# Kernel tuning notes

Hardware: AMD Instinct MI355X
Metric: run time of the kernel (lower is better)

## Reference

```python
import jax, jax.numpy as jnp
import numpy as np

B, S, H, NH = 1, 4096, 1024, 16
HD = H // NH  # 64


def _rope_tables(seq_len, dim):
    inv_freq = 1.0 / (10000.0 ** (np.arange(0, dim, 2, dtype=np.float32) / dim))
    t = np.arange(seq_len, dtype=np.float32)
    freqs = np.outer(t, inv_freq)                 # [S, dim/2]
    emb = np.concatenate([freqs, freqs], axis=-1)  # [S, dim]
    return jnp.asarray(np.cos(emb)), jnp.asarray(np.sin(emb))


def setup_inputs() -> dict:
    key = jax.random.key(0)
    ks = jax.random.split(key, 5)
    hidden_states = jax.random.normal(ks[0], (B, S, H), dtype=jnp.float32)
    scale = 1.0 / np.sqrt(H)
    Wq = jax.random.normal(ks[1], (H, H), dtype=jnp.float32) * scale
    Wk = jax.random.normal(ks[2], (H, H), dtype=jnp.float32) * scale
    Wv = jax.random.normal(ks[3], (H, H), dtype=jnp.float32) * scale
    Wo = jax.random.normal(ks[4], (H, H), dtype=jnp.float32) * scale
    cos, sin = _rope_tables(S, HD)
    # additive causal mask [1,1,S,S]
    causal = jnp.where(
        jnp.tril(jnp.ones((S, S), dtype=bool)), 0.0, jnp.float32(-1e9)
    )[None, None]
    return {
        "hidden_states": hidden_states,
        "cos": cos,
        "sin": sin,
        "attention_mask": causal,
        "Wq": Wq,
        "Wk": Wk,
        "Wv": Wv,
        "Wo": Wo,
    }


def _rotate_half(x):
    x1, x2 = jnp.split(x, 2, axis=-1)
    return jnp.concatenate([-x2, x1], axis=-1)


def _apply_rope(q, k, cos, sin):
    # q,k: [B,NH,S,HD]; cos/sin: [S,HD] -> broadcast [1,1,S,HD]
    cos = cos[None, None]
    sin = sin[None, None]
    q = q * cos + _rotate_half(q) * sin
    k = k * cos + _rotate_half(k) * sin
    return q, k


def reference(hidden_states, cos, sin, attention_mask, Wq, Wk, Wv, Wo):
    bsz, q_len, _ = hidden_states.shape
    q = hidden_states @ Wq.T
    k = hidden_states @ Wk.T
    v = hidden_states @ Wv.T
    # [B,S,H] -> [B,NH,S,HD]
    def split_heads(x):
        return x.reshape(bsz, q_len, NH, HD).transpose(0, 2, 1, 3)
    q, k, v = split_heads(q), split_heads(k), split_heads(v)
    q, k = _apply_rope(q, k, cos, sin)
    scores = jnp.einsum("bhqd,bhkd->bhqk", q, k) / jnp.sqrt(jnp.float32(HD))
    scores = scores + attention_mask
    attn = jax.nn.softmax(scores, axis=-1)
    out = jnp.einsum("bhqk,bhkd->bhqd", attn, v)
    out = out.transpose(0, 2, 1, 3).reshape(bsz, q_len, H)
    return out @ Wo.T
```

## Files before the change

kernel.cpp:

```cpp
#include <hip/hip_runtime.h>

#define S_LEN 4096
#define NHEADS 16
#define HD 64
#define HDIM 1024

typedef __attribute__((ext_vector_type(8))) __bf16 bf16x8;
typedef __attribute__((ext_vector_type(4))) float f32x4;
typedef __attribute__((ext_vector_type(4))) int i32x4;
typedef unsigned short u16;

static __device__ __forceinline__ u16 f2bu(float f) {
    unsigned u = __builtin_bit_cast(unsigned, f);
    u += 0x7FFFu + ((u >> 16) & 1u);
    return (u16)(u >> 16);
}
static __device__ __forceinline__ int pack_bf16(float lo, float hi) {
    return (int)__builtin_amdgcn_perm(__builtin_bit_cast(unsigned, hi),
                                      __builtin_bit_cast(unsigned, lo), 0x07060302u);
}
static __device__ __forceinline__ float fexp2(float x) {
    return __builtin_amdgcn_exp2f(x);
}

static __device__ __forceinline__ bf16x8 read_frag(const u16* lds, int row, int kbyte) {
    int c = kbyte ^ ((row & 7) << 4);
    return *reinterpret_cast<const bf16x8*>(reinterpret_cast<const char*>(lds) + row * 128 + c);
}
static __device__ __forceinline__ bf16x8 read_off(const u16* lds, int byteoff) {
    return *reinterpret_cast<const bf16x8*>(reinterpret_cast<const char*>(lds) + byteoff);
}

static __device__ __forceinline__ void stage_gll(const u16* __restrict__ src, const u16* lds, unsigned ldsbyte) {
    __builtin_amdgcn_global_load_lds(
        (const __attribute__((address_space(1))) void*)src,
        (__attribute__((address_space(3))) void*)(reinterpret_cast<const char*>(lds) + ldsbyte),
        16, 0, 0);
}

static __device__ __forceinline__ void softmax_gather(
    const f32x4* sf, float& l_part, bf16x8* pf, int lj, int lc)
{
    int pk[4][2];
#pragma unroll
    for (int nf = 0; nf < 4; ++nf) {
        float p0 = fexp2(sf[nf][0]);
        float p1 = fexp2(sf[nf][1]);
        float p2 = fexp2(sf[nf][2]);
        float p3 = fexp2(sf[nf][3]);
        l_part += (p0 + p1) + (p2 + p3);
        pk[nf][0] = pack_bf16(p0, p1);
        pk[nf][1] = pack_bf16(p2, p3);
    }
#pragma unroll
    for (int kb = 0; kb < 2; ++kb) {
        i32x4 u;
#pragma unroll
        for (int s = 0; s < 4; ++s) {
            int srcl = lc + (((2 * lj + (s >> 1)) & 3) << 4);
            int v0 = __shfl(pk[2 * kb][s & 1], srcl);
            int v1 = __shfl(pk[2 * kb + 1][s & 1], srcl);
            u[s] = (lj & 2) ? v1 : v0;
        }
        pf[kb] = __builtin_bit_cast(bf16x8, u);
    }
}

__global__ __launch_bounds__(256) void cvt_all(
    const float* __restrict__ X, const float* __restrict__ Wq, const float* __restrict__ Wk,
    const float* __restrict__ Wv, const float* __restrict__ Wo,
    u16* __restrict__ Xb, u16* __restrict__ Wqb, u16* __restrict__ Wkb,
    u16* __restrict__ Wvb, u16* __restrict__ Wob)
{
    int i = blockIdx.x * 256 + threadIdx.x;
    const float* src; u16* dst; int off;
    if (i < (1 << 20)) { src = X; dst = Xb; off = i; }
    else {
        int j = i - (1 << 20);
        int w = j >> 18; off = j & 0x3FFFF;
        src = (w == 0) ? Wq : (w == 1) ? Wk : (w == 2) ? Wv : Wo;
        dst = (w == 0) ? Wqb : (w == 1) ? Wkb : (w == 2) ? Wvb : Wob;
    }
    float4 v = reinterpret_cast<const float4*>(src)[off];
    ushort4 o;
    o.x = f2bu(v.x); o.y = f2bu(v.y); o.z = f2bu(v.z); o.w = f2bu(v.w);
    reinterpret_cast<ushort4*>(dst)[off] = o;
}

__global__ __launch_bounds__(256) void qkv_gemm(
    const u16* __restrict__ A,
    const u16* __restrict__ Wq, const u16* __restrict__ Wk, const u16* __restrict__ Wv,
    u16* __restrict__ Qb, u16* __restrict__ Kb, u16* __restrict__ VTb,
    const float* __restrict__ cosT, const float* __restrict__ sinT)
{
    __shared__ u16 At[128 * 64];
    __shared__ u16 Bt[128 * 64];
    const int z = blockIdx.z;
    const u16* W = (z == 0) ? Wq : (z == 1) ? Wk : Wv;
    const int tid = threadIdx.x;
    const int wid = tid >> 6, lane = tid & 63;
    const int wm = wid >> 1, wn = wid & 1;
    const int lj = lane >> 4, lc = lane & 15;
    const int m0 = blockIdx.y * 128, n0 = blockIdx.x * 128;

    f32x4 acc[4][4];
#pragma unroll
    for (int i = 0; i < 4; ++i)
#pragma unroll
        for (int j = 0; j < 4; ++j) acc[i][j] = 0.0f;

    for (int k0 = 0; k0 < HDIM; k0 += 64) {
        __syncthreads();
#pragma unroll
        for (int r = 0; r < 4; ++r) {
            int idx = (r << 8) + tid;
            int row = idx >> 3;
            int c = (idx & 7) << 4;
            int csw = c ^ ((row & 7) << 4);
            unsigned lb = (unsigned)(idx & ~63) << 4;
            stage_gll(A + (size_t)(m0 + row) * HDIM + k0 + (csw >> 1), At, lb);
            stage_gll(W + (size_t)(n0 + row) * HDIM + k0 + (csw >> 1), Bt, lb);
        }
        __syncthreads();
#pragma unroll
        for (int kb = 0; kb < 2; ++kb) {
            int kbyte = (kb << 6) + (lj << 4);
            bf16x8 af[4], bfr[4];
#pragma unroll
            for (int mf = 0; mf < 4; ++mf) af[mf] = read_frag(At, (wm << 6) + (mf << 4) + lc, kbyte);
#pragma unroll
            for (int nf = 0; nf < 4; ++nf) bfr[nf] = read_frag(Bt, (wn << 6) + (nf << 4) + lc, kbyte);
#pragma unroll
            for (int mf = 0; mf < 4; ++mf)
#pragma unroll
                for (int nf = 0; nf < 4; ++nf)
                    acc[mf][nf] = __builtin_amdgcn_mfma_f32_16x16x32_bf16(af[mf], bfr[nf], acc[mf][nf], 0, 0, 0);
        }
    }

    const int mrow0 = m0 + (wm << 6);
    const int ncol0 = n0 + (wn << 6);
    if (z == 2) {
#pragma unroll
        for (int mf = 0; mf < 4; ++mf)
#pragma unroll
            for (int nf = 0; nf < 4; ++nf)
#pragma unroll
                for (int j = 0; j < 4; ++j) {
                    int s = mrow0 + (mf << 4) + (lj << 2) + j;
                    int o = ncol0 + (nf << 4) + lc;
                    VTb[((size_t)(o >> 6) * HD + (o & 63)) * S_LEN + s] = f2bu(acc[mf][nf][j]);
                }
    } else {
        u16* outB = (z == 0) ? Qb : Kb;
        const float sc = (z == 0) ? 0.18033688011112042f : 1.0f;
#pragma unroll
        for (int mf = 0; mf < 4; ++mf) {
            float nv[4][4];
#pragma unroll
            for (int nf = 0; nf < 4; ++nf)
#pragma unroll
                for (int j = 0; j < 4; ++j) {
                    int s = mrow0 + (mf << 4) + (lj << 2) + j;
                    int o = ncol0 + (nf << 4) + lc;
                    int d = o & 63;
                    float x  = acc[mf][nf][j];
                    float xp = acc[mf][nf ^ 2][j];
                    float cv = cosT[(size_t)s * HD + d];
                    float sv = sinT[(size_t)s * HD + d];
                    float rot = (d < 32) ? -xp : xp;
                    nv[nf][j] = (x * cv + rot * sv) * sc;
                }
#pragma unroll
            for (int nf = 0; nf < 4; ++nf)
#pragma unroll
                for (int j = 0; j < 4; ++j) {
                    int s = mrow0 + (mf << 4) + (lj << 2) + j;
                    int o = ncol0 + (nf << 4) + lc;
                    outB[((size_t)(o >> 6) * S_LEN + s) * HD + (o & 63)] = f2bu(nv[nf][j]);
                }
        }
    }
}

__global__ __launch_bounds__(256) void wo_gemm(
    const u16* __restrict__ A, const u16* __restrict__ W, float* __restrict__ outF)
{
    __shared__ u16 At[128 * 64];
    __shared__ u16 Bt[64 * 64];
    const int tid = threadIdx.x;
    const int wid = tid >> 6, lane = tid & 63;
    const int wm = wid >> 1, wn = wid & 1;
    const int lj = lane >> 4, lc = lane & 15;
    const int m0 = blockIdx.y * 128, n0 = blockIdx.x * 64;

    f32x4 acc[4][2];
#pragma unroll
    for (int i = 0; i < 4; ++i)
#pragma unroll
        for (int j = 0; j < 2; ++j) acc[i][j] = 0.0f;

    for (int k0 = 0; k0 < HDIM; k0 += 64) {
        __syncthreads();
#pragma unroll
        for (int r = 0; r < 4; ++r) {
            int idx = (r << 8) + tid;
            int row = idx >> 3;
            int c = (idx & 7) << 4;
            int csw = c ^ ((row & 7) << 4);
            unsigned lb = (unsigned)(idx & ~63) << 4;
            stage_gll(A + (size_t)(m0 + row) * HDIM + k0 + (csw >> 1), At, lb);
            if (r < 2)
                stage_gll(W + (size_t)(n0 + row) * HDIM + k0 + (csw >> 1), Bt, lb);
        }
        __syncthreads();
#pragma unroll
        for (int kb = 0; kb < 2; ++kb) {
            int kbyte = (kb << 6) + (lj << 4);
            bf16x8 af[4], bfr[2];
#pragma unroll
            for (int mf = 0; mf < 4; ++mf) af[mf] = read_frag(At, (wm << 6) + (mf << 4) + lc, kbyte);
#pragma unroll
            for (int nf = 0; nf < 2; ++nf) bfr[nf] = read_frag(Bt, (wn << 5) + (nf << 4) + lc, kbyte);
#pragma unroll
            for (int mf = 0; mf < 4; ++mf)
#pragma unroll
                for (int nf = 0; nf < 2; ++nf)
                    acc[mf][nf] = __builtin_amdgcn_mfma_f32_16x16x32_bf16(af[mf], bfr[nf], acc[mf][nf], 0, 0, 0);
        }
    }

    const int mrow0 = m0 + (wm << 6);
    const int ncol0 = n0 + (wn << 5);
#pragma unroll
    for (int mf = 0; mf < 4; ++mf)
#pragma unroll
        for (int nf = 0; nf < 2; ++nf)
#pragma unroll
            for (int j = 0; j < 4; ++j) {
                int s = mrow0 + (mf << 4) + (lj << 2) + j;
                int o = ncol0 + (nf << 4) + lc;
                outF[(size_t)s * HDIM + o] = acc[mf][nf][j];
            }
}

__global__ __launch_bounds__(256, 2) void attn_fwd(
    const u16* __restrict__ Q, const u16* __restrict__ K,
    const u16* __restrict__ VT, u16* __restrict__ AO)
{
    __shared__ u16 Kt[2][128 * 64];
    __shared__ u16 Vt[2][2][64 * 64];

    const int tid = threadIdx.x;
    const int wid = tid >> 6, lane = tid & 63;
    const int lj = lane >> 4, lc = lane & 15;

    const int lid = blockIdx.x;
    const int x = lid & 7, g = lid >> 3;
    const int a = g >> 5, c = g & 31;
    const int b = a ? (31 - c) : c;
    const int h = (x << 1) | a;
    const int qtA = 63 - b, qtB = b;
    const int qbaseA = qtA * 64 + wid * 16;
    const int qbaseB = qtB * 64 + wid * 16;
    const int nsteps = qtA + 1;

    const u16* Qh = Q + (size_t)h * S_LEN * HD;

    const int srow = tid >> 3;
    const int csw  = ((tid & 7) << 4) ^ ((srow & 7) << 4);
    const u16* kbase = K  + (size_t)h * S_LEN * HD + (size_t)srow * HD + (csw >> 1);
    const u16* vbase = VT + (size_t)h * HD * S_LEN + (size_t)srow * S_LEN + (csw >> 1);
    const unsigned lb = (unsigned)(tid & ~63) << 4;

#define SK(buf, hf, t) do { \
        const u16* p_ = kbase + (size_t)(t) * 64 * HD; \
        stage_gll(p_,           (const u16*)Kt[buf] + (hf) * 4096, lb); \
        stage_gll(p_ + 32 * HD, (const u16*)Kt[buf] + (hf) * 4096, lb + 4096); \
    } while (0)
#define SV(buf, hf, t) do { \
        const u16* p_ = vbase + (t) * 64; \
        stage_gll(p_,              (const u16*)Vt[buf][hf], lb); \
        stage_gll(p_ + 32 * S_LEN, (const u16*)Vt[buf][hf], lb + 4096); \
    } while (0)

    int foff[2][4];
#pragma unroll
    for (int kb = 0; kb < 2; ++kb)
#pragma unroll
        for (int nf = 0; nf < 4; ++nf) {
            int row = (nf << 4) + lc;
            foff[kb][nf] = row * 128 + (((kb << 6) + (lj << 4)) ^ ((row & 7) << 4));
        }

    bf16x8 qB0[2], qB1[2];
#pragma unroll
    for (int kb = 0; kb < 2; ++kb) {
        qB0[kb] = *reinterpret_cast<const bf16x8*>(
            Qh + (size_t)(qbaseA + lc) * HD + (kb << 5) + (lj << 3));
        qB1[kb] = *reinterpret_cast<const bf16x8*>(
            Qh + (size_t)(qbaseB + lc) * HD + (kb << 5) + (lj << 3));
    }

    f32x4 accO0[4], accO1[4];
    float l0 = 0.0f, l1 = 0.0f;
#pragma unroll
    for (int df = 0; df < 4; ++df) { accO0[df] = 0.0f; accO1[df] = 0.0f; }

    bf16x8 pf0[2], pf1[2], vf[2][4];

    auto compute = [&](int t, const u16* KtH, const u16* VtH) {
        const bool act1 = (t <= qtB);
        const bool pv1  = (t >= 1) && (t <= qtB + 1);

        bf16x8 kf[2][4];
#pragma unroll
        for (int kb = 0; kb < 2; ++kb)
#pragma unroll
            for (int nf = 0; nf < 4; ++nf)
                kf[kb][nf] = read_off(KtH, foff[kb][nf]);

        f32x4 sf0[4], sf1[4];
#pragma unroll
        for (int nf = 0; nf < 4; ++nf) { sf0[nf] = 0.0f; sf1[nf] = 0.0f; }

        __builtin_amdgcn_s_setprio(1);
#pragma unroll
        for (int kb = 0; kb < 2; ++kb)
#pragma unroll
            for (int nf = 0; nf < 4; ++nf)
                sf0[nf] = __builtin_amdgcn_mfma_f32_16x16x32_bf16(kf[kb][nf], qB0[kb], sf0[nf], 0, 0, 0);
        if (act1) {
#pragma unroll
            for (int kb = 0; kb < 2; ++kb)
#pragma unroll
                for (int nf = 0; nf < 4; ++nf)
                    sf1[nf] = __builtin_amdgcn_mfma_f32_16x16x32_bf16(kf[kb][nf], qB1[kb], sf1[nf], 0, 0, 0);
        }
        if (t >= 1) {
#pragma unroll
            for (int kb = 0; kb < 2; ++kb)
#pragma unroll
                for (int df = 0; df < 4; ++df)
                    accO0[df] = __builtin_amdgcn_mfma_f32_16x16x32_bf16(pf0[kb], vf[kb][df], accO0[df], 0, 0, 0);
        }
        if (pv1) {
#pragma unroll
            for (int kb = 0; kb < 2; ++kb)
#pragma unroll
                for (int df = 0; df < 4; ++df)
                    accO1[df] = __builtin_amdgcn_mfma_f32_16x16x32_bf16(pf1[kb], vf[kb][df], accO1[df], 0, 0, 0);
        }
        __builtin_amdgcn_s_setprio(0);

#pragma unroll
        for (int kb = 0; kb < 2; ++kb)
#pragma unroll
            for (int df = 0; df < 4; ++df)
                vf[kb][df] = read_off(VtH, foff[kb][df]);

        const int kv0 = t << 6;
        if (t == qtA) {
            int qg = qbaseA + lc;
#pragma unroll
            for (int nf = 0; nf < 4; ++nf)
#pragma unroll
                for (int j = 0; j < 4; ++j) {
                    int kvg = kv0 + (nf << 4) + (lj << 2) + j;
                    if (kvg > qg) sf0[nf][j] = -1e30f;
                }
        }
        if (act1 && t == qtB) {
            int qg = qbaseB + lc;
#pragma unroll
            for (int nf = 0; nf < 4; ++nf)
#pragma unroll
                for (int j = 0; j < 4; ++j) {
                    int kvg = kv0 + (nf << 4) + (lj << 2) + j;
                    if (kvg > qg) sf1[nf][j] = -1e30f;
                }
        }

        softmax_gather(sf0, l0, pf0, lj, lc);
        if (act1) softmax_gather(sf1, l1, pf1, lj, lc);
    };

    SK(0, 0, 0); SV(0, 0, 0);
    if (nsteps > 1) { SK(0, 1, 1); SV(0, 1, 1); }
    __syncthreads();

    const int nmac = (nsteps + 1) >> 1;
    int cur = 0;
    for (int m = 0; m < nmac; ++m) {
        const int t2 = 2 * m + 2, t3 = 2 * m + 3;
        if (t2 < nsteps) { SK(cur ^ 1, 0, t2); SV(cur ^ 1, 0, t2); }
        if (t3 < nsteps) { SK(cur ^ 1, 1, t3); SV(cur ^ 1, 1, t3); }

        compute(2 * m, (const u16*)Kt[cur], (const u16*)Vt[cur][0]);
        if (2 * m + 1 < nsteps)
            compute(2 * m + 1, (const u16*)Kt[cur] + 4096, (const u16*)Vt[cur][1]);

        __syncthreads();
        cur ^= 1;
    }

#pragma unroll
    for (int kb = 0; kb < 2; ++kb)
#pragma unroll
        for (int df = 0; df < 4; ++df)
            accO0[df] = __builtin_amdgcn_mfma_f32_16x16x32_bf16(pf0[kb], vf[kb][df], accO0[df], 0, 0, 0);

    l0 += __shfl_xor(l0, 16); l0 += __shfl_xor(l0, 32);
    l1 += __shfl_xor(l1, 16); l1 += __shfl_xor(l1, 32);
    float lr0[4], lr1[4];
#pragma unroll
    for (int j = 0; j < 4; ++j) {
        lr0[j] = __shfl(l0, (lj << 2) + j);
        lr1[j] = __shfl(l1, (lj << 2) + j);
    }
#pragma unroll
    for (int df = 0; df < 4; ++df)
#pragma unroll
        for (int j = 0; j < 4; ++j) {
            int sA = qbaseA + (lj << 2) + j;
            int sB = qbaseB + (lj << 2) + j;
            int d = (df << 4) + lc;
            AO[(size_t)sA * HDIM + h * HD + d] = f2bu(accO0[df][j] / lr0[j]);
            AO[(size_t)sB * HDIM + h * HD + d] = f2bu(accO1[df][j] / lr1[j]);
        }
#undef SK
#undef SV
}

extern "C" void kernel_launch(void* const* d_in, const int* in_sizes, int n_in,
                              void* d_out, int out_size, void* d_ws, size_t ws_size,
                              hipStream_t stream) {
    const float* hidden = (const float*)d_in[0];
    const float* cosT   = (const float*)d_in[1];
    const float* sinT   = (const float*)d_in[2];
    const float* Wq = (const float*)d_in[4];
    const float* Wk = (const float*)d_in[5];
    const float* Wv = (const float*)d_in[6];
    const float* Wo = (const float*)d_in[7];
    float* out = (float*)d_out;

    char* ws = (char*)d_ws;
    u16* Xb  = (u16*)(ws);
    u16* Wqb = (u16*)(ws + (size_t)( 8 << 20));
    u16* Wkb = (u16*)(ws + (size_t)(10 << 20));
    u16* Wvb = (u16*)(ws + (size_t)(12 << 20));
    u16* Wob = (u16*)(ws + (size_t)(14 << 20));
    u16* Qb  = (u16*)(ws + (size_t)(16 << 20));
    u16* Kb  = (u16*)(ws + (size_t)(24 << 20));
    u16* VTb = (u16*)(ws + (size_t)(32 << 20));
    u16* AOb = (u16*)(ws + (size_t)(40 << 20));

    cvt_all<<<8192, 256, 0, stream>>>(hidden, Wq, Wk, Wv, Wo, Xb, Wqb, Wkb, Wvb, Wob);

    qkv_gemm<<<dim3(HDIM / 128, S_LEN / 128, 3), 256, 0, stream>>>(
        Xb, Wqb, Wkb, Wvb, Qb, Kb, VTb, cosT, sinT);

    attn_fwd<<<dim3(512), 256, 0, stream>>>(Qb, Kb, VTb, AOb);

    wo_gemm<<<dim3(HDIM / 64, S_LEN / 128), 256, 0, stream>>>(AOb, Wob, out);
}
```

Measured before the change: 165.2 us.

## Replace double-buffered pair staging with triple-buffered per-tile pipeline

Replaces the double-buffered scheme, which loaded two KV tiles per macro-step, with a three-slot ring buffer that loads one 64-row K/V tile per step, prefetched two steps ahead. Each step waits with a partial vmcnt on the outstanding global-to-LDS loads and takes one barrier per tile, so the next loads stay in flight while the current tile is computed. LDS use drops slightly (three 64x64 slots instead of two 128x64). The cost is one barrier per tile instead of one per two tiles. Correctness relies on the hand-set vmcnt count matching the number of load instructions issued per stage, and on nsteps==1 issuing an SK(1,1) load for a tile that may be out of range.

```diff
diff --git a/kernel.cpp b/kernel.cpp
--- a/kernel.cpp
+++ b/kernel.cpp
@@ -248,8 +248,8 @@
     const u16* __restrict__ Q, const u16* __restrict__ K,
     const u16* __restrict__ VT, u16* __restrict__ AO)
 {
-    __shared__ u16 Kt[2][128 * 64];
-    __shared__ u16 Vt[2][2][64 * 64];
+    __shared__ u16 Kt[3][64 * 64];
+    __shared__ u16 Vt[3][64 * 64];
 
     const int tid = threadIdx.x;
     const int wid = tid >> 6, lane = tid & 63;
@@ -273,15 +273,15 @@
     const u16* vbase = VT + (size_t)h * HD * S_LEN + (size_t)srow * S_LEN + (csw >> 1);
     const unsigned lb = (unsigned)(tid & ~63) << 4;
 
-#define SK(buf, hf, t) do { \
+#define SK(buf, t) do { \
         const u16* p_ = kbase + (size_t)(t) * 64 * HD; \
-        stage_gll(p_,           (const u16*)Kt[buf] + (hf) * 4096, lb); \
-        stage_gll(p_ + 32 * HD, (const u16*)Kt[buf] + (hf) * 4096, lb + 4096); \
+        stage_gll(p_,           (const u16*)Kt[buf], lb); \
+        stage_gll(p_ + 32 * HD, (const u16*)Kt[buf], lb + 4096); \
     } while (0)
-#define SV(buf, hf, t) do { \
+#define SV(buf, t) do { \
         const u16* p_ = vbase + (t) * 64; \
-        stage_gll(p_,              (const u16*)Vt[buf][hf], lb); \
-        stage_gll(p_ + 32 * S_LEN, (const u16*)Vt[buf][hf], lb + 4096); \
+        stage_gll(p_,              (const u16*)Vt[buf], lb); \
+        stage_gll(p_ + 32 * S_LEN, (const u16*)Vt[buf], lb + 4096); \
     } while (0)
 
     int foff[2][4];
@@ -385,23 +385,25 @@
         if (act1) softmax_gather(sf1, l1, pf1, lj, lc);
     };
 
-    SK(0, 0, 0); SV(0, 0, 0);
-    if (nsteps > 1) { SK(0, 1, 1); SV(0, 1, 1); }
-    __syncthreads();
-
-    const int nmac = (nsteps + 1) >> 1;
-    int cur = 0;
-    for (int m = 0; m < nmac; ++m) {
-        const int t2 = 2 * m + 2, t3 = 2 * m + 3;
-        if (t2 < nsteps) { SK(cur ^ 1, 0, t2); SV(cur ^ 1, 0, t2); }
-        if (t3 < nsteps) { SK(cur ^ 1, 1, t3); SV(cur ^ 1, 1, t3); }
-
-        compute(2 * m, (const u16*)Kt[cur], (const u16*)Vt[cur][0]);
-        if (2 * m + 1 < nsteps)
-            compute(2 * m + 1, (const u16*)Kt[cur] + 4096, (const u16*)Vt[cur][1]);
-
-        __syncthreads();
-        cur ^= 1;
+    SK(0, 0); SV(0, 0);
+    SK(1, 1); SV(1, 1);
+
+    for (int t = 0; t < nsteps; ++t) {
+        if (t == nsteps - 1) {
+            asm volatile("s_waitcnt vmcnt(0) lgkmcnt(0)" ::: "memory");
+        } else {
+            asm volatile("s_waitcnt vmcnt(4) lgkmcnt(0)" ::: "memory");
+        }
+        __builtin_amdgcn_sched_barrier(0);
+        __builtin_amdgcn_s_barrier();
+        __builtin_amdgcn_sched_barrier(0);
+
+        if (t + 2 < nsteps) {
+            const int nb = (t + 2) % 3;
+            SK(nb, t + 2); SV(nb, t + 2);
+        }
+
+        compute(t, (const u16*)Kt[t % 3], (const u16*)Vt[t % 3]);
     }
 
 #pragma unroll
```

Result: slower. 177.2 us (+7.3%).
